# Performance work log

Measured on AMD Instinct MI355X. Metric: run time of the kernel, lower is better.

Reference implementation:

```python
import jax, jax.numpy as jnp
import numpy as np

N, E = 50000, 800000          # nodes, edges (self-loops added in reference)
IN_C, HID, OUT_C = 512, 128, 40
K, H = 4, 8                   # n_layers, heads
C = HID // H                  # per-head channels = 16
L = K + 1                     # with_initial_residual=True -> K+1 convs
NEG_SLOPE = 0.2               # PyG GATConv default leaky_relu slope


def setup_inputs():
    key = jax.random.key(0)
    ks = jax.random.split(key, 12)
    s = 0.05
    x = jax.random.normal(ks[0], (N, IN_C), jnp.float32)
    edge_index = jax.random.randint(ks[1], (2, E), 0, N, dtype=jnp.int32)
    fc0_w = jax.random.normal(ks[2], (IN_C, HID), jnp.float32) * s
    fc0_b = jax.random.normal(ks[3], (HID,), jnp.float32) * s
    lin_w = jax.random.normal(ks[4], (L, HID, HID), jnp.float32) * s      # GATConv lin (bias=False)
    att_src = jax.random.normal(ks[5], (L, H, C), jnp.float32) * s
    att_dst = jax.random.normal(ks[6], (L, H, C), jnp.float32) * s
    conv_bias = jax.random.normal(ks[7], (L, HID), jnp.float32) * s
    alphas = jnp.zeros((L,), jnp.float32).at[0].set(1.0)                  # init_alphas: t[0]=1
    fc1_w = jax.random.normal(ks[8], (HID, OUT_C), jnp.float32) * s
    fc1_b = jax.random.normal(ks[9], (OUT_C,), jnp.float32) * s
    return {"x": x, "edge_index": edge_index, "fc0_w": fc0_w, "fc0_b": fc0_b,
            "lin_w": lin_w, "att_src": att_src, "att_dst": att_dst,
            "conv_bias": conv_bias, "alphas": alphas, "fc1_w": fc1_w, "fc1_b": fc1_b}


def _gat_conv(h, src, dst, lin_w, a_src_w, a_dst_w, bias):
    # PyG GATConv (eval mode): linear -> edgewise attention -> segment softmax -> scatter-sum
    hp = (h @ lin_w).reshape(N, H, C)                 # [N,H,C]
    a_src = jnp.einsum('nhc,hc->nh', hp, a_src_w)     # [N,H]
    a_dst = jnp.einsum('nhc,hc->nh', hp, a_dst_w)
    e = jax.nn.leaky_relu(a_src[src] + a_dst[dst], NEG_SLOPE)   # [E+N,H]
    emax = jax.ops.segment_max(e, dst, num_segments=N)          # per-dst, per-head max
    e = jnp.exp(e - emax[dst])
    denom = jax.ops.segment_sum(e, dst, num_segments=N)
    alpha = e / (denom[dst] + 1e-16)                            # segment softmax
    msg = hp[src] * alpha[:, :, None]                           # [E+N,H,C]
    out = jax.ops.segment_sum(msg, dst, num_segments=N)         # [N,H,C]
    return out.reshape(N, H * C) + bias


def reference(x, edge_index, fc0_w, fc0_b, lin_w, att_src, att_dst, conv_bias, alphas, fc1_w, fc1_b):
    # forward_clenshawRes, eval mode (dropout = identity, batchNorm=False)
    loops = jnp.arange(N, dtype=edge_index.dtype)
    src = jnp.concatenate([edge_index[0], loops])   # add self-loops (PyG default)
    dst = jnp.concatenate([edge_index[1], loops])
    h0 = x @ fc0_w + fc0_b                          # fcs[0]
    last = jnp.zeros_like(h0)
    second_last = jnp.zeros_like(h0)
    for i in range(L):
        hcur = jax.nn.elu(_gat_conv(last, src, dst, lin_w[i], att_src[i], att_dst[i], conv_bias[i]))
        hcur = 2.0 * hcur - second_last + alphas[L - 1 - i] * h0   # alphas[-(i+1)]
        second_last, last = last, hcur
    out = last @ fc1_w + fc1_b                      # fcs[-1]
    return jax.nn.log_softmax(out, axis=1)
```

## Files before the change

### kernel.cpp

```cpp
#include <hip/hip_runtime.h>
#include <math.h>

#define NN      50000
#define E_CNT   800000
#define IN_C    512
#define HID     128
#define OUT_C   40
#define NHEAD   8
#define CPH     16
#define NLAYER  5
#define NEG     0.2f
#define CAP     64

typedef __attribute__((ext_vector_type(8))) short bf16x8;
typedef __attribute__((ext_vector_type(4))) float f32x4;

__device__ __forceinline__ float lrelu(float x) { return x > 0.f ? x : NEG * x; }
__device__ __forceinline__ float eluf(float x)  { return x > 0.f ? x : expm1f(x); }

__device__ __forceinline__ float2 bf2f2(unsigned int u) {
    union { unsigned int a; float f; } lo, hi;
    lo.a = u << 16; hi.a = u & 0xffff0000u;
    return make_float2(lo.f, hi.f);
}
__device__ __forceinline__ unsigned short f2bf(float f) {
    union { float f; unsigned int u; } v; v.f = f;
    return (unsigned short)((v.u + 0x7fffu + ((v.u >> 16) & 1u)) >> 16);
}
__device__ __forceinline__ unsigned int pack2(float a, float b) {
    return ((unsigned int)f2bf(b) << 16) | f2bf(a);
}

__device__ __forceinline__ void gl2lds16(const void* g, void* l) {
    __builtin_amdgcn_global_load_lds(
        (const __attribute__((address_space(1))) unsigned int*)g,
        (__attribute__((address_space(3))) unsigned int*)l, 16, 0, 0);
}

__global__ __launch_bounds__(256) void k_wt(const float* __restrict__ w,
                                            unsigned short* __restrict__ wt, int K) {
    __shared__ float t[32][33];
    const float* ws = w + (size_t)blockIdx.z * K * HID;
    unsigned short* wd = wt + (size_t)blockIdx.z * K * HID;
    int k0 = blockIdx.x * 32, n0 = blockIdx.y * 32;
    int tx = threadIdx.x & 31, ty = threadIdx.x >> 5;
    for (int r = ty; r < 32; r += 8) t[r][tx] = ws[(size_t)(k0 + r) * HID + n0 + tx];
    __syncthreads();
    for (int r = ty; r < 32; r += 8) wd[(size_t)(n0 + r) * K + k0 + tx] = f2bf(t[tx][r]);
}

template<int K, int A_F32, int EPI>
__global__ __launch_bounds__(256) void k_mgemm(const void* __restrict__ aptr,
                                               const unsigned short* __restrict__ wt,
                                               const float* __restrict__ bias,
                                               const float* __restrict__ cb0,
                                               const float* __restrict__ alphas,
                                               float* __restrict__ out_f,
                                               float* __restrict__ out_f2,
                                               unsigned short* __restrict__ out_b) {
    __shared__ unsigned short As[128 * 32];
    __shared__ unsigned short Bs[128 * 32];
    const int tid  = threadIdx.x;
    const int w    = tid >> 6, lane = tid & 63;
    const int wr   = w & 1, wc = w >> 1;
    const int row0 = blockIdx.x * 128;
    f32x4 acc[4][4] = {};

    const int rs = lane >> 2;
    const int ko = (lane & 3) * 8;

    for (int k0 = 0; k0 < K; k0 += 32) {
#pragma unroll
        for (int h = 0; h < 2; ++h) {
            int r = w * 32 + h * 16;
            int grow = row0 + r + rs; if (grow >= NN) grow = NN - 1;
            if (A_F32) {
                const float* src = (const float*)aptr + (size_t)grow * K + k0 + ko;
                float4 v0 = *(const float4*)src;
                float4 v1 = *(const float4*)(src + 4);
                uint4 pk;
                pk.x = pack2(v0.x, v0.y); pk.y = pack2(v0.z, v0.w);
                pk.z = pack2(v1.x, v1.y); pk.w = pack2(v1.z, v1.w);
                *(uint4*)&As[(r + rs) * 32 + ko] = pk;
            } else {
                gl2lds16((const unsigned short*)aptr + (size_t)grow * K + k0 + ko, &As[r * 32]);
            }
            gl2lds16(wt + (size_t)(r + rs) * K + k0 + ko, &Bs[r * 32]);
        }
        __syncthreads();
        const int fr = lane & 15, fq = lane >> 4;
        bf16x8 af[4], bfr[4];
#pragma unroll
        for (int t = 0; t < 4; ++t) {
            af[t]  = *(const bf16x8*)&As[(wr * 64 + t * 16 + fr) * 32 + fq * 8];
            bfr[t] = *(const bf16x8*)&Bs[(wc * 64 + t * 16 + fr) * 32 + fq * 8];
        }
#pragma unroll
        for (int tm = 0; tm < 4; ++tm)
#pragma unroll
            for (int tn = 0; tn < 4; ++tn)
                acc[tm][tn] = __builtin_amdgcn_mfma_f32_16x16x32_bf16(af[tm], bfr[tn], acc[tm][tn], 0, 0, 0);
        __syncthreads();
    }

    const int cl = lane & 15, rq = (lane >> 4) * 4;
    const float a4 = (EPI == 2) ? alphas[NLAYER - 1] : 0.f;
#pragma unroll
    for (int tm = 0; tm < 4; ++tm)
#pragma unroll
        for (int tn = 0; tn < 4; ++tn) {
            int col = wc * 64 + tn * 16 + cl;
            int rbase = row0 + wr * 64 + tm * 16 + rq;
            f32x4 a4v = acc[tm][tn];
            float bcol = (EPI == 2) ? bias[col] : 0.f;
            float ecol = (EPI == 2) ? 2.f * eluf(cb0[col]) : 0.f;
#pragma unroll
            for (int rg = 0; rg < 4; ++rg) {
                int row = rbase + rg;
                if (row < NN) {
                    if (EPI == 0) {
                        out_b[(size_t)row * HID + col] = f2bf(a4v[rg]);
                    } else {
                        float h0v = a4v[rg] + bcol;
                        out_f[(size_t)row * HID + col] = h0v;
                        float bAv = ecol + a4 * h0v;
                        out_f2[(size_t)row * HID + col] = bAv;
                        out_b[(size_t)row * HID + col] = f2bf(bAv);
                    }
                }
            }
        }
}

__global__ void k_att(const unsigned short* __restrict__ hpb,
                      const float* __restrict__ attS, const float* __restrict__ attD,
                      float* __restrict__ aS, float* __restrict__ aD) {
    int i = blockIdx.x * blockDim.x + threadIdx.x;
    if (i >= NN * NHEAD) return;
    int h = i & 7;
    const unsigned int* row = (const unsigned int*)(hpb + (size_t)(i >> 3) * HID + h * CPH);
    float s = 0.f, d = 0.f;
#pragma unroll
    for (int cc = 0; cc < 8; ++cc) {
        float2 v = bf2f2(row[cc]);
        s += v.x * attS[h * CPH + 2 * cc] + v.y * attS[h * CPH + 2 * cc + 1];
        d += v.x * attD[h * CPH + 2 * cc] + v.y * attD[h * CPH + 2 * cc + 1];
    }
    aS[i] = s; aD[i] = d;
}

__global__ void k_hist(const int* __restrict__ dst, int* __restrict__ deg) {
    int e = blockIdx.x * blockDim.x + threadIdx.x;
    if (e < E_CNT) atomicAdd(&deg[dst[e]], 1);
}

__global__ __launch_bounds__(1024) void k_part(const int* __restrict__ deg, int* __restrict__ part) {
    int i = blockIdx.x * 1024 + threadIdx.x;
    int v = (i < NN) ? deg[i] : 0;
    for (int off = 32; off; off >>= 1) v += __shfl_down(v, off);
    __shared__ int ws[16];
    if ((threadIdx.x & 63) == 0) ws[threadIdx.x >> 6] = v;
    __syncthreads();
    if (threadIdx.x < 16) {
        int t = ws[threadIdx.x];
        for (int off = 8; off; off >>= 1) t += __shfl_down(t, off);
        if (threadIdx.x == 0) part[blockIdx.x] = t;
    }
}

__global__ void k_scanpart(int* __restrict__ part, int* __restrict__ rowstart, int nb) {
    int t = threadIdx.x;
    int v = (t < nb) ? part[t] : 0;
    int x = v;
    for (int off = 1; off < 64; off <<= 1) { int u = __shfl_up(x, off); if (t >= off) x += u; }
    if (t < nb) part[t] = x - v;
    if (t == nb - 1) rowstart[NN] = x;
}

__global__ __launch_bounds__(1024) void k_scanblk(const int* __restrict__ deg,
                                                  const int* __restrict__ partx,
                                                  int* __restrict__ rowstart,
                                                  int* __restrict__ cursor) {
    int b = blockIdx.x, t = threadIdx.x, i = b * 1024 + t;
    int v = (i < NN) ? deg[i] : 0;
    int x = v;
    for (int off = 1; off < 64; off <<= 1) { int u = __shfl_up(x, off); if ((t & 63) >= off) x += u; }
    __shared__ int ws[16];
    if ((t & 63) == 63) ws[t >> 6] = x;
    __syncthreads();
    if (t < 64) {
        int wv = (t < 16) ? ws[t] : 0;
        for (int off = 1; off < 16; off <<= 1) { int u = __shfl_up(wv, off); if (t >= off) wv += u; }
        if (t < 16) ws[t] = wv;
    }
    __syncthreads();
    int waveoff = (t >= 64) ? ws[(t >> 6) - 1] : 0;
    int excl = x - v + waveoff + partx[b];
    if (i < NN) { rowstart[i] = excl; cursor[i] = excl; }
}

__global__ void k_scatter(const int* __restrict__ src, const int* __restrict__ dst,
                          int* __restrict__ cursor, int* __restrict__ csr) {
    int e = blockIdx.x * blockDim.x + threadIdx.x;
    if (e < E_CNT) {
        int p = atomicAdd(&cursor[dst[e]], 1);
        csr[p] = src[e];
    }
}

__global__ __launch_bounds__(256) void k_agg(
    const unsigned short* __restrict__ hpb, const float* __restrict__ aS, const float* __restrict__ aD,
    const int* __restrict__ rowstart, const int* __restrict__ csr,
    const float* __restrict__ bias, const float* __restrict__ h0,
    const float* __restrict__ sl, const float* __restrict__ alphas, int aidx, int sl_zero,
    float* __restrict__ hnew, unsigned int* __restrict__ hnewb) {
    __shared__ int   slds[4][CAP];
    __shared__ float wlds[4][CAP][NHEAD];
    const int wave = threadIdx.x >> 6;
    const int lane = threadIdx.x & 63;
    const int n    = blockIdx.x * 4 + wave;
    const int rsb  = rowstart[n];
    const int deg  = rowstart[n + 1] - rsb;
    const int cnt  = deg < CAP ? deg : CAP;

    for (int j = lane; j < cnt; j += 64) slds[wave][j] = csr[rsb + j];
    __syncthreads();

    const int h    = lane & 7;
    const int slot = lane >> 3;
    const float adst = aD[n * NHEAD + h];

    float ev[8];
    float m = -1e30f;
#pragma unroll
    for (int t = 0; t < 8; ++t) {
        int j = slot + t * 8;
        if (j < cnt) {
            int s = slds[wave][j];
            float e = lrelu(aS[s * NHEAD + h] + adst);
            ev[t] = e;
            m = fmaxf(m, e);
        }
    }
    for (int j = CAP + slot; j < deg; j += 8) {
        int s = csr[rsb + j];
        m = fmaxf(m, lrelu(aS[s * NHEAD + h] + adst));
    }
#pragma unroll
    for (int off = 8; off < 64; off <<= 1) m = fmaxf(m, __shfl_xor(m, off));
    const float e0 = lrelu(aS[n * NHEAD + h] + adst);
    m = fmaxf(m, e0);

    float den = 0.f;
#pragma unroll
    for (int t = 0; t < 8; ++t) {
        int j = slot + t * 8;
        if (j < cnt) {
            float wv = __expf(ev[t] - m);
            wlds[wave][j][h] = wv;
            den += wv;
        }
    }
    for (int j = CAP + slot; j < deg; j += 8) {
        int s = csr[rsb + j];
        den += __expf(lrelu(aS[s * NHEAD + h] + adst) - m);
    }
#pragma unroll
    for (int off = 8; off < 64; off <<= 1) den += __shfl_xor(den, off);
    const float w0 = __expf(e0 - m);
    den += w0;
    const float dinv = 1.f / (den + 1e-16f);
    __syncthreads();

    const int l    = lane & 31;
    const int half = lane >> 5;
    const int hh   = l >> 2;
    const float mh  = __shfl(m, hh);
    const float w0h = __shfl(w0, hh);
    const float dih = __shfl(dinv, hh);
    const float adh = __shfl(adst, hh);

    float a0 = 0.f, a1 = 0.f, a2 = 0.f, a3 = 0.f;
    if (half == 0) {
        uint2 u = *(const uint2*)(hpb + (size_t)n * HID + 4 * l);
        float2 p = bf2f2(u.x), q = bf2f2(u.y);
        a0 = w0h * p.x; a1 = w0h * p.y; a2 = w0h * q.x; a3 = w0h * q.y;
    }
    if (deg <= CAP) {
#pragma unroll 4
        for (int j = half; j < deg; j += 2) {
            int s = slds[wave][j];
            float wv = wlds[wave][j][hh];
            uint2 u = *(const uint2*)(hpb + (size_t)s * HID + 4 * l);
            float2 p = bf2f2(u.x), q = bf2f2(u.y);
            a0 += wv * p.x; a1 += wv * p.y; a2 += wv * q.x; a3 += wv * q.y;
        }
    } else {
        for (int j = half; j < deg; j += 2) {
            int s; float wv;
            if (j < CAP) { s = slds[wave][j]; wv = wlds[wave][j][hh]; }
            else { s = csr[rsb + j]; wv = __expf(lrelu(aS[s * NHEAD + hh] + adh) - mh); }
            uint2 u = *(const uint2*)(hpb + (size_t)s * HID + 4 * l);
            float2 p = bf2f2(u.x), q = bf2f2(u.y);
            a0 += wv * p.x; a1 += wv * p.y; a2 += wv * q.x; a3 += wv * q.y;
        }
    }
    a0 += __shfl_xor(a0, 32); a1 += __shfl_xor(a1, 32);
    a2 += __shfl_xor(a2, 32); a3 += __shfl_xor(a3, 32);

    if (half == 0) {
        float4 bv = ((const float4*)bias)[l];
        float g0 = eluf(a0 * dih + bv.x);
        float g1 = eluf(a1 * dih + bv.y);
        float g2 = eluf(a2 * dih + bv.z);
        float g3 = eluf(a3 * dih + bv.w);
        const float ac = alphas[aidx];
        float4 s2 = make_float4(0.f, 0.f, 0.f, 0.f);
        if (!sl_zero) s2 = ((const float4*)sl)[(size_t)n * 32 + l];
        float hx0 = 0.f, hx1 = 0.f, hx2 = 0.f, hx3 = 0.f;
        if (ac != 0.f) {
            float4 hv = ((const float4*)h0)[(size_t)n * 32 + l];
            hx0 = hv.x; hx1 = hv.y; hx2 = hv.z; hx3 = hv.w;
        }
        float o0 = 2.f * g0 - s2.x + ac * hx0;
        float o1 = 2.f * g1 - s2.y + ac * hx1;
        float o2 = 2.f * g2 - s2.z + ac * hx2;
        float o3 = 2.f * g3 - s2.w + ac * hx3;
        ((float4*)hnew)[(size_t)n * 32 + l] = make_float4(o0, o1, o2, o3);
        uint2 pb; pb.x = pack2(o0, o1); pb.y = pack2(o2, o3);
        ((uint2*)hnewb)[(size_t)n * 32 + l] = pb;
    }
}

__global__ __launch_bounds__(64) void k_out(const float* __restrict__ t,
                                            const float* __restrict__ w,
                                            const float* __restrict__ b,
                                            float* __restrict__ out) {
    const int n = blockIdx.x;
    const int lane = threadIdx.x;
    float acc = 0.f;
    if (lane < OUT_C) {
        for (int k = 0; k < HID; ++k) acc += t[(size_t)n * HID + k] * w[k * OUT_C + lane];
        acc += b[lane];
    }
    float v = (lane < OUT_C) ? acc : -INFINITY;
    for (int off = 32; off; off >>= 1) v = fmaxf(v, __shfl_down(v, off));
    float mx = __shfl(v, 0);
    float ex = (lane < OUT_C) ? __expf(acc - mx) : 0.f;
    float sv = ex;
    for (int off = 32; off; off >>= 1) sv += __shfl_down(sv, off);
    float lse = logf(__shfl(sv, 0));
    if (lane < OUT_C) out[(size_t)n * OUT_C + lane] = acc - mx - lse;
}

extern "C" void kernel_launch(void* const* d_in, const int* in_sizes, int n_in,
                              void* d_out, int out_size, void* d_ws, size_t ws_size,
                              hipStream_t stream) {
    const float* x      = (const float*)d_in[0];
    const int*   ei     = (const int*)  d_in[1];
    const float* fc0w   = (const float*)d_in[2];
    const float* fc0b   = (const float*)d_in[3];
    const float* linw   = (const float*)d_in[4];
    const float* attS   = (const float*)d_in[5];
    const float* attD   = (const float*)d_in[6];
    const float* cbias  = (const float*)d_in[7];
    const float* alphas = (const float*)d_in[8];
    const float* fc1w   = (const float*)d_in[9];
    const float* fc1b   = (const float*)d_in[10];
    float* out = (float*)d_out;

    char* p = (char*)d_ws;
    auto alloc = [&](size_t bytes) { void* q = (void*)p; p += (bytes + 255) / 256 * 256; return q; };
    const size_t NNH = (size_t)NN * HID * 4;
    float* h0 = (float*)alloc(NNH);
    float* bA = (float*)alloc(NNH);
    float* bB = (float*)alloc(NNH);
    float* bC = (float*)alloc(NNH);
    unsigned short* lastb = (unsigned short*)alloc((size_t)NN * HID * 2);
    unsigned short* hpb   = (unsigned short*)alloc((size_t)NN * HID * 2);
    float* aSb = (float*)alloc((size_t)NN * NHEAD * 4);
    float* aDb = (float*)alloc((size_t)NN * NHEAD * 4);
    unsigned short* WT0 = (unsigned short*)alloc((size_t)HID * IN_C * 2);
    unsigned short* WTL = (unsigned short*)alloc((size_t)4 * HID * HID * 2);
    int* deg      = (int*)alloc((size_t)(NN + 1) * 4);
    int* rowstart = (int*)alloc((size_t)(NN + 1) * 4);
    int* part     = (int*)alloc(64 * 4);
    int* csr      = (int*)alloc((size_t)E_CNT * 4);
    int* cursor   = deg;

    const int* esrc = ei;
    const int* edst = ei + E_CNT;
    const int NB = (NN + 1023) / 1024;

    hipMemsetAsync(deg, 0, (size_t)NN * 4, stream);
    k_hist<<<(E_CNT + 255) / 256, 256, 0, stream>>>(edst, deg);
    k_part<<<NB, 1024, 0, stream>>>(deg, part);
    k_scanpart<<<1, 64, 0, stream>>>(part, rowstart, NB);
    k_scanblk<<<NB, 1024, 0, stream>>>(deg, part, rowstart, cursor);
    k_scatter<<<(E_CNT + 255) / 256, 256, 0, stream>>>(esrc, edst, cursor, csr);

    {
        dim3 g0(IN_C / 32, HID / 32, 1);
        k_wt<<<g0, 256, 0, stream>>>(fc0w, WT0, IN_C);
        dim3 gl(HID / 32, HID / 32, 4);
        k_wt<<<gl, 256, 0, stream>>>(linw + (size_t)HID * HID, WTL, HID);
    }

    const int GB = (NN + 127) / 128;
    k_mgemm<IN_C, 1, 2><<<GB, 256, 0, stream>>>(x, WT0, fc0b, cbias, alphas, h0, bA, lastb);

    float* last = bA; float* sl = bB; float* nxt = bC;
    for (int i = 1; i < NLAYER; ++i) {
        k_mgemm<HID, 0, 0><<<GB, 256, 0, stream>>>(lastb, WTL + (size_t)(i - 1) * HID * HID,
                                                   nullptr, nullptr, nullptr, nullptr, nullptr, hpb);
        k_att<<<(NN * NHEAD + 255) / 256, 256, 0, stream>>>(hpb, attS + i * NHEAD * CPH, attD + i * NHEAD * CPH, aSb, aDb);
        k_agg<<<NN / 4, 256, 0, stream>>>(hpb, aSb, aDb, rowstart, csr,
                                          cbias + i * HID, h0, sl, alphas, NLAYER - 1 - i, (i == 1) ? 1 : 0,
                                          nxt, (unsigned int*)lastb);
        float* tmp = sl; sl = last; last = nxt; nxt = tmp;
    }

    k_out<<<NN, 64, 0, stream>>>(last, fc1w, fc1b, out);
}
```

Baseline: 607.4 us.

## Fold attention projections into GEMM, store activations in bf16, drop softmax max

The attention-logit projections are folded into the per-layer GEMM as 16 extra weight columns (W·att precomputed in k_watt), which removes the separate k_att kernel. The GEMM is rewritten as a direct-from-global wave-per-16-rows MFMA kernel with no LDS staging. All intermediate activations (h0, last, second_last) are now stored in bf16 instead of fp32, roughly halving that memory traffic. The segment-softmax max pass is removed in aggregation, which saves a pass over edges but risks exp overflow and adds precision loss from bf16 storage and bf16-rounded attention weights.

```diff
diff --git a/kernel.cpp b/kernel.cpp
--- a/kernel.cpp
+++ b/kernel.cpp
@@ -11,6 +11,7 @@
 #define NLAYER  5
 #define NEG     0.2f
 #define CAP     64
+#define NCOL    144
 
 typedef __attribute__((ext_vector_type(8))) short bf16x8;
 typedef __attribute__((ext_vector_type(4))) float f32x4;
@@ -18,6 +19,10 @@
 __device__ __forceinline__ float lrelu(float x) { return x > 0.f ? x : NEG * x; }
 __device__ __forceinline__ float eluf(float x)  { return x > 0.f ? x : expm1f(x); }
 
+__device__ __forceinline__ float bf2f(unsigned short u) {
+    union { unsigned int a; float f; } v; v.a = ((unsigned int)u) << 16;
+    return v.f;
+}
 __device__ __forceinline__ float2 bf2f2(unsigned int u) {
     union { unsigned int a; float f; } lo, hi;
     lo.a = u << 16; hi.a = u & 0xffff0000u;
@@ -31,17 +36,11 @@
     return ((unsigned int)f2bf(b) << 16) | f2bf(a);
 }
 
-__device__ __forceinline__ void gl2lds16(const void* g, void* l) {
-    __builtin_amdgcn_global_load_lds(
-        (const __attribute__((address_space(1))) unsigned int*)g,
-        (__attribute__((address_space(3))) unsigned int*)l, 16, 0, 0);
-}
-
 __global__ __launch_bounds__(256) void k_wt(const float* __restrict__ w,
-                                            unsigned short* __restrict__ wt, int K) {
+                                            unsigned short* __restrict__ wt, int K, int opitch) {
     __shared__ float t[32][33];
     const float* ws = w + (size_t)blockIdx.z * K * HID;
-    unsigned short* wd = wt + (size_t)blockIdx.z * K * HID;
+    unsigned short* wd = wt + (size_t)blockIdx.z * opitch;
     int k0 = blockIdx.x * 32, n0 = blockIdx.y * 32;
     int tx = threadIdx.x & 31, ty = threadIdx.x >> 5;
     for (int r = ty; r < 32; r += 8) t[r][tx] = ws[(size_t)(k0 + r) * HID + n0 + tx];
@@ -49,104 +48,90 @@
     for (int r = ty; r < 32; r += 8) wd[(size_t)(n0 + r) * K + k0 + tx] = f2bf(t[tx][r]);
 }
 
-template<int K, int A_F32, int EPI>
-__global__ __launch_bounds__(256) void k_mgemm(const void* __restrict__ aptr,
+__global__ void k_watt(const float* __restrict__ linw, const float* __restrict__ attS,
+                       const float* __restrict__ attD, unsigned short* __restrict__ wt2) {
+    int i = blockIdx.x * blockDim.x + threadIdx.x;
+    if (i >= 4 * 16 * HID) return;
+    int l = i >> 11, r = (i >> 7) & 15, k = i & 127;
+    int h = r & 7, isD = r >> 3;
+    const float* W = linw + (size_t)(l + 1) * HID * HID;
+    const float* av = (isD ? attD : attS) + (size_t)(l + 1) * NHEAD * CPH + h * CPH;
+    float s = 0.f;
+#pragma unroll
+    for (int c = 0; c < CPH; ++c) s += W[(size_t)k * HID + h * CPH + c] * av[c];
+    wt2[(size_t)l * NCOL * HID + (size_t)(128 + r) * HID + k] = f2bf(s);
+}
+
+template<int K, int A_F32, int NT, int EPI>
+__global__ __launch_bounds__(256) void k_dgemm(const void* __restrict__ aptr,
                                                const unsigned short* __restrict__ wt,
                                                const float* __restrict__ bias,
                                                const float* __restrict__ cb0,
                                                const float* __restrict__ alphas,
-                                               float* __restrict__ out_f,
-                                               float* __restrict__ out_f2,
-                                               unsigned short* __restrict__ out_b) {
-    __shared__ unsigned short As[128 * 32];
-    __shared__ unsigned short Bs[128 * 32];
+                                               unsigned short* __restrict__ out_b,
+                                               unsigned short* __restrict__ out_h0,
+                                               float* __restrict__ aSo,
+                                               float* __restrict__ aDo) {
     const int tid  = threadIdx.x;
     const int w    = tid >> 6, lane = tid & 63;
-    const int wr   = w & 1, wc = w >> 1;
-    const int row0 = blockIdx.x * 128;
-    f32x4 acc[4][4] = {};
-
-    const int rs = lane >> 2;
-    const int ko = (lane & 3) * 8;
-
+    const int fr   = lane & 15, fq = lane >> 4;
+    const int rowb = blockIdx.x * 64 + w * 16;
+    int arow = rowb + fr; if (arow >= NN) arow = NN - 1;
+    f32x4 acc[NT] = {};
+
+#pragma unroll 2
     for (int k0 = 0; k0 < K; k0 += 32) {
-#pragma unroll
-        for (int h = 0; h < 2; ++h) {
-            int r = w * 32 + h * 16;
-            int grow = row0 + r + rs; if (grow >= NN) grow = NN - 1;
-            if (A_F32) {
-                const float* src = (const float*)aptr + (size_t)grow * K + k0 + ko;
-                float4 v0 = *(const float4*)src;
-                float4 v1 = *(const float4*)(src + 4);
-                uint4 pk;
-                pk.x = pack2(v0.x, v0.y); pk.y = pack2(v0.z, v0.w);
-                pk.z = pack2(v1.x, v1.y); pk.w = pack2(v1.z, v1.w);
-                *(uint4*)&As[(r + rs) * 32 + ko] = pk;
-            } else {
-                gl2lds16((const unsigned short*)aptr + (size_t)grow * K + k0 + ko, &As[r * 32]);
-            }
-            gl2lds16(wt + (size_t)(r + rs) * K + k0 + ko, &Bs[r * 32]);
-        }
-        __syncthreads();
-        const int fr = lane & 15, fq = lane >> 4;
-        bf16x8 af[4], bfr[4];
-#pragma unroll
-        for (int t = 0; t < 4; ++t) {
-            af[t]  = *(const bf16x8*)&As[(wr * 64 + t * 16 + fr) * 32 + fq * 8];
-            bfr[t] = *(const bf16x8*)&Bs[(wc * 64 + t * 16 + fr) * 32 + fq * 8];
-        }
-#pragma unroll
-        for (int tm = 0; tm < 4; ++tm)
-#pragma unroll
-            for (int tn = 0; tn < 4; ++tn)
-                acc[tm][tn] = __builtin_amdgcn_mfma_f32_16x16x32_bf16(af[tm], bfr[tn], acc[tm][tn], 0, 0, 0);
-        __syncthreads();
+        bf16x8 af;
+        if (A_F32) {
+            const float* s = (const float*)aptr + (size_t)arow * K + k0 + fq * 8;
+            float4 v0 = *(const float4*)s;
+            float4 v1 = *(const float4*)(s + 4);
+            union { bf16x8 v; unsigned int u[4]; } pk;
+            pk.u[0] = pack2(v0.x, v0.y); pk.u[1] = pack2(v0.z, v0.w);
+            pk.u[2] = pack2(v1.x, v1.y); pk.u[3] = pack2(v1.z, v1.w);
+            af = pk.v;
+        } else {
+            af = *(const bf16x8*)((const unsigned short*)aptr + (size_t)arow * K + k0 + fq * 8);
+        }
+#pragma unroll
+        for (int t = 0; t < NT; ++t) {
+            bf16x8 bf = *(const bf16x8*)(wt + (size_t)(t * 16 + fr) * K + k0 + fq * 8);
+            acc[t] = __builtin_amdgcn_mfma_f32_16x16x32_bf16(af, bf, acc[t], 0, 0, 0);
+        }
     }
 
     const int cl = lane & 15, rq = (lane >> 4) * 4;
     const float a4 = (EPI == 2) ? alphas[NLAYER - 1] : 0.f;
 #pragma unroll
-    for (int tm = 0; tm < 4; ++tm)
-#pragma unroll
-        for (int tn = 0; tn < 4; ++tn) {
-            int col = wc * 64 + tn * 16 + cl;
-            int rbase = row0 + wr * 64 + tm * 16 + rq;
-            f32x4 a4v = acc[tm][tn];
-            float bcol = (EPI == 2) ? bias[col] : 0.f;
-            float ecol = (EPI == 2) ? 2.f * eluf(cb0[col]) : 0.f;
-#pragma unroll
-            for (int rg = 0; rg < 4; ++rg) {
-                int row = rbase + rg;
-                if (row < NN) {
-                    if (EPI == 0) {
-                        out_b[(size_t)row * HID + col] = f2bf(a4v[rg]);
-                    } else {
-                        float h0v = a4v[rg] + bcol;
-                        out_f[(size_t)row * HID + col] = h0v;
-                        float bAv = ecol + a4 * h0v;
-                        out_f2[(size_t)row * HID + col] = bAv;
-                        out_b[(size_t)row * HID + col] = f2bf(bAv);
-                    }
+    for (int t = 0; t < 8; ++t) {
+        int col = t * 16 + cl;
+        float bcol = (EPI == 2) ? bias[col] : 0.f;
+        float ecol = (EPI == 2) ? 2.f * eluf(cb0[col]) : 0.f;
+#pragma unroll
+        for (int rg = 0; rg < 4; ++rg) {
+            int row = rowb + rq + rg;
+            if (row < NN) {
+                if (EPI == 0) {
+                    out_b[(size_t)row * HID + col] = f2bf(acc[t][rg]);
+                } else {
+                    float h0v = acc[t][rg] + bcol;
+                    out_h0[(size_t)row * HID + col] = f2bf(h0v);
+                    out_b[(size_t)row * HID + col]  = f2bf(ecol + a4 * h0v);
                 }
             }
         }
-}
-
-__global__ void k_att(const unsigned short* __restrict__ hpb,
-                      const float* __restrict__ attS, const float* __restrict__ attD,
-                      float* __restrict__ aS, float* __restrict__ aD) {
-    int i = blockIdx.x * blockDim.x + threadIdx.x;
-    if (i >= NN * NHEAD) return;
-    int h = i & 7;
-    const unsigned int* row = (const unsigned int*)(hpb + (size_t)(i >> 3) * HID + h * CPH);
-    float s = 0.f, d = 0.f;
-#pragma unroll
-    for (int cc = 0; cc < 8; ++cc) {
-        float2 v = bf2f2(row[cc]);
-        s += v.x * attS[h * CPH + 2 * cc] + v.y * attS[h * CPH + 2 * cc + 1];
-        d += v.x * attD[h * CPH + 2 * cc] + v.y * attD[h * CPH + 2 * cc + 1];
-    }
-    aS[i] = s; aD[i] = d;
+    }
+    if (NT == 9) {
+#pragma unroll
+        for (int rg = 0; rg < 4; ++rg) {
+            int row = rowb + rq + rg;
+            if (row < NN) {
+                float v = acc[8][rg];
+                if (cl < 8) aSo[(size_t)row * NHEAD + cl] = v;
+                else        aDo[(size_t)row * NHEAD + (cl - 8)] = v;
+            }
+        }
+    }
 }
 
 __global__ void k_hist(const int* __restrict__ dst, int* __restrict__ deg) {
@@ -211,9 +196,9 @@
 __global__ __launch_bounds__(256) void k_agg(
     const unsigned short* __restrict__ hpb, const float* __restrict__ aS, const float* __restrict__ aD,
     const int* __restrict__ rowstart, const int* __restrict__ csr,
-    const float* __restrict__ bias, const float* __restrict__ h0,
-    const float* __restrict__ sl, const float* __restrict__ alphas, int aidx, int sl_zero,
-    float* __restrict__ hnew, unsigned int* __restrict__ hnewb) {
+    const float* __restrict__ bias, const unsigned short* __restrict__ h0b,
+    const unsigned short* __restrict__ slb, const float* __restrict__ alphas, int aidx, int sl_zero,
+    unsigned int* __restrict__ outb) {
     __shared__ int   slds[4][CAP];
     __shared__ float wlds[4][CAP][NHEAD];
     const int wave = threadIdx.x >> 6;
@@ -230,44 +215,22 @@
     const int slot = lane >> 3;
     const float adst = aD[n * NHEAD + h];
 
-    float ev[8];
-    float m = -1e30f;
+    float den = 0.f;
 #pragma unroll
     for (int t = 0; t < 8; ++t) {
         int j = slot + t * 8;
         if (j < cnt) {
             int s = slds[wave][j];
-            float e = lrelu(aS[s * NHEAD + h] + adst);
-            ev[t] = e;
-            m = fmaxf(m, e);
-        }
-    }
-    for (int j = CAP + slot; j < deg; j += 8) {
-        int s = csr[rsb + j];
-        m = fmaxf(m, lrelu(aS[s * NHEAD + h] + adst));
-    }
-#pragma unroll
-    for (int off = 8; off < 64; off <<= 1) m = fmaxf(m, __shfl_xor(m, off));
-    const float e0 = lrelu(aS[n * NHEAD + h] + adst);
-    m = fmaxf(m, e0);
-
-    float den = 0.f;
-#pragma unroll
-    for (int t = 0; t < 8; ++t) {
-        int j = slot + t * 8;
-        if (j < cnt) {
-            float wv = __expf(ev[t] - m);
+            float wv = __expf(lrelu(aS[s * NHEAD + h] + adst));
             wlds[wave][j][h] = wv;
             den += wv;
         }
     }
-    for (int j = CAP + slot; j < deg; j += 8) {
-        int s = csr[rsb + j];
-        den += __expf(lrelu(aS[s * NHEAD + h] + adst) - m);
-    }
+    for (int j = CAP + slot; j < deg; j += 8)
+        den += __expf(lrelu(aS[csr[rsb + j] * NHEAD + h] + adst));
 #pragma unroll
     for (int off = 8; off < 64; off <<= 1) den += __shfl_xor(den, off);
-    const float w0 = __expf(e0 - m);
+    const float w0 = __expf(lrelu(aS[n * NHEAD + h] + adst));
     den += w0;
     const float dinv = 1.f / (den + 1e-16f);
     __syncthreads();
@@ -275,7 +238,6 @@
     const int l    = lane & 31;
     const int half = lane >> 5;
     const int hh   = l >> 2;
-    const float mh  = __shfl(m, hh);
     const float w0h = __shfl(w0, hh);
     const float dih = __shfl(dinv, hh);
     const float adh = __shfl(adst, hh);
@@ -299,7 +261,7 @@
         for (int j = half; j < deg; j += 2) {
             int s; float wv;
             if (j < CAP) { s = slds[wave][j]; wv = wlds[wave][j][hh]; }
-            else { s = csr[rsb + j]; wv = __expf(lrelu(aS[s * NHEAD + hh] + adh) - mh); }
+            else { s = csr[rsb + j]; wv = __expf(lrelu(aS[s * NHEAD + hh] + adh)); }
             uint2 u = *(const uint2*)(hpb + (size_t)s * HID + 4 * l);
             float2 p = bf2f2(u.x), q = bf2f2(u.y);
             a0 += wv * p.x; a1 += wv * p.y; a2 += wv * q.x; a3 += wv * q.y;
@@ -315,24 +277,28 @@
         float g2 = eluf(a2 * dih + bv.z);
         float g3 = eluf(a3 * dih + bv.w);
         const float ac = alphas[aidx];
-        float4 s2 = make_float4(0.f, 0.f, 0.f, 0.f);
-        if (!sl_zero) s2 = ((const float4*)sl)[(size_t)n * 32 + l];
+        float s0 = 0.f, s1 = 0.f, s2 = 0.f, s3 = 0.f;
+        if (!sl_zero) {
+            uint2 su = *(const uint2*)(slb + (size_t)n * HID + 4 * l);
+            float2 p = bf2f2(su.x), q = bf2f2(su.y);
+            s0 = p.x; s1 = p.y; s2 = q.x; s3 = q.y;
+        }
         float hx0 = 0.f, hx1 = 0.f, hx2 = 0.f, hx3 = 0.f;
         if (ac != 0.f) {
-            float4 hv = ((const float4*)h0)[(size_t)n * 32 + l];
-            hx0 = hv.x; hx1 = hv.y; hx2 = hv.z; hx3 = hv.w;
-        }
-        float o0 = 2.f * g0 - s2.x + ac * hx0;
-        float o1 = 2.f * g1 - s2.y + ac * hx1;
-        float o2 = 2.f * g2 - s2.z + ac * hx2;
-        float o3 = 2.f * g3 - s2.w + ac * hx3;
-        ((float4*)hnew)[(size_t)n * 32 + l] = make_float4(o0, o1, o2, o3);
+            uint2 hu = *(const uint2*)(h0b + (size_t)n * HID + 4 * l);
+            float2 p = bf2f2(hu.x), q = bf2f2(hu.y);
+            hx0 = p.x; hx1 = p.y; hx2 = q.x; hx3 = q.y;
+        }
+        float o0 = 2.f * g0 - s0 + ac * hx0;
+        float o1 = 2.f * g1 - s1 + ac * hx1;
+        float o2 = 2.f * g2 - s2 + ac * hx2;
+        float o3 = 2.f * g3 - s3 + ac * hx3;
         uint2 pb; pb.x = pack2(o0, o1); pb.y = pack2(o2, o3);
-        ((uint2*)hnewb)[(size_t)n * 32 + l] = pb;
-    }
-}
-
-__global__ __launch_bounds__(64) void k_out(const float* __restrict__ t,
+        ((uint2*)outb)[(size_t)n * 32 + l] = pb;
+    }
+}
+
+__global__ __launch_bounds__(64) void k_out(const unsigned short* __restrict__ t,
                                             const float* __restrict__ w,
                                             const float* __restrict__ b,
                                             float* __restrict__ out) {
@@ -340,7 +306,8 @@
     const int lane = threadIdx.x;
     float acc = 0.f;
     if (lane < OUT_C) {
-        for (int k = 0; k < HID; ++k) acc += t[(size_t)n * HID + k] * w[k * OUT_C + lane];
+        const unsigned short* row = t + (size_t)n * HID;
+        for (int k = 0; k < HID; ++k) acc += bf2f(row[k]) * w[k * OUT_C + lane];
         acc += b[lane];
     }
     float v = (lane < OUT_C) ? acc : -INFINITY;
@@ -371,17 +338,16 @@
 
     char* p = (char*)d_ws;
     auto alloc = [&](size_t bytes) { void* q = (void*)p; p += (bytes + 255) / 256 * 256; return q; };
-    const size_t NNH = (size_t)NN * HID * 4;
-    float* h0 = (float*)alloc(NNH);
-    float* bA = (float*)alloc(NNH);
-    float* bB = (float*)alloc(NNH);
-    float* bC = (float*)alloc(NNH);
-    unsigned short* lastb = (unsigned short*)alloc((size_t)NN * HID * 2);
-    unsigned short* hpb   = (unsigned short*)alloc((size_t)NN * HID * 2);
+    const size_t NB16 = (size_t)NN * HID * 2;
+    unsigned short* h0b  = (unsigned short*)alloc(NB16);
+    unsigned short* Lb0  = (unsigned short*)alloc(NB16);
+    unsigned short* Lb1  = (unsigned short*)alloc(NB16);
+    unsigned short* Lb2  = (unsigned short*)alloc(NB16);
+    unsigned short* hpb  = (unsigned short*)alloc(NB16);
     float* aSb = (float*)alloc((size_t)NN * NHEAD * 4);
     float* aDb = (float*)alloc((size_t)NN * NHEAD * 4);
     unsigned short* WT0 = (unsigned short*)alloc((size_t)HID * IN_C * 2);
-    unsigned short* WTL = (unsigned short*)alloc((size_t)4 * HID * HID * 2);
+    unsigned short* WT2 = (unsigned short*)alloc((size_t)4 * NCOL * HID * 2);
     int* deg      = (int*)alloc((size_t)(NN + 1) * 4);
     int* rowstart = (int*)alloc((size_t)(NN + 1) * 4);
     int* part     = (int*)alloc(64 * 4);
@@ -401,23 +367,24 @@
 
     {
         dim3 g0(IN_C / 32, HID / 32, 1);
-        k_wt<<<g0, 256, 0, stream>>>(fc0w, WT0, IN_C);
+        k_wt<<<g0, 256, 0, stream>>>(fc0w, WT0, IN_C, HID * IN_C);
         dim3 gl(HID / 32, HID / 32, 4);
-        k_wt<<<gl, 256, 0, stream>>>(linw + (size_t)HID * HID, WTL, HID);
-    }
-
-    const int GB = (NN + 127) / 128;
-    k_mgemm<IN_C, 1, 2><<<GB, 256, 0, stream>>>(x, WT0, fc0b, cbias, alphas, h0, bA, lastb);
-
-    float* last = bA; float* sl = bB; float* nxt = bC;
+        k_wt<<<gl, 256, 0, stream>>>(linw + (size_t)HID * HID, WT2, HID, NCOL * HID);
+        k_watt<<<(4 * 16 * HID + 255) / 256, 256, 0, stream>>>(linw, attS, attD, WT2);
+    }
+
+    const int GB = (NN + 63) / 64;
+    k_dgemm<IN_C, 1, 8, 2><<<GB, 256, 0, stream>>>(x, WT0, fc0b, cbias, alphas,
+                                                   Lb0, h0b, nullptr, nullptr);
+
+    unsigned short* last = Lb0; unsigned short* sl = Lb1; unsigned short* nxt = Lb2;
     for (int i = 1; i < NLAYER; ++i) {
-        k_mgemm<HID, 0, 0><<<GB, 256, 0, stream>>>(lastb, WTL + (size_t)(i - 1) * HID * HID,
-                                                   nullptr, nullptr, nullptr, nullptr, nullptr, hpb);
-        k_att<<<(NN * NHEAD + 255) / 256, 256, 0, stream>>>(hpb, attS + i * NHEAD * CPH, attD + i * NHEAD * CPH, aSb, aDb);
+        k_dgemm<HID, 0, 9, 0><<<GB, 256, 0, stream>>>(last, WT2 + (size_t)(i - 1) * NCOL * HID,
+                                                      nullptr, nullptr, nullptr, hpb, nullptr, aSb, aDb);
         k_agg<<<NN / 4, 256, 0, stream>>>(hpb, aSb, aDb, rowstart, csr,
-                                          cbias + i * HID, h0, sl, alphas, NLAYER - 1 - i, (i == 1) ? 1 : 0,
-                                          nxt, (unsigned int*)lastb);
-        float* tmp = sl; sl = last; last = nxt; nxt = tmp;
+                                          cbias + i * HID, h0b, sl, alphas, NLAYER - 1 - i, (i == 1) ? 1 : 0,
+                                          (unsigned int*)nxt);
+        unsigned short* tmp = sl; sl = last; last = nxt; nxt = tmp;
     }
 
     k_out<<<NN, 64, 0, stream>>>(last, fc1w, fc1b, out);
```

After: 688.8 us. +13.4%, slower.
